# Optimization experiments

Measured on AMD Instinct MI355X. Metric: run time of the kernel, lower is better.

Reference implementation:

```python
import jax, jax.numpy as jnp
import numpy as np
import math

B, C, BINS, W = 2, 8, 1024, 512
HEADS = 16
HD = BINS // HEADS          # 64 head dim
ROT = BINS // HEADS // 2    # 32 rotated dims
EXP = 4
EPS = 1e-5
MAX_FREQ = 10.0


def setup_inputs() -> dict:
    key = jax.random.key(0)
    ks = jax.random.split(key, 8)
    def u(k, shape, fan_in):
        lim = 1.0 / math.sqrt(fan_in)
        return jax.random.uniform(k, shape, jnp.float32, -lim, lim)
    return {
        "x": jax.random.normal(ks[0], (B, C, BINS, W), jnp.float32),
        "norm1_w": jnp.ones((BINS,), jnp.float32),
        "norm1_b": jnp.zeros((BINS,), jnp.float32),
        # 'pixel' rotary init: linspace(1, max_freq/2, dim//2) * pi (learned)
        "rot_freqs": jnp.linspace(1.0, MAX_FREQ / 2, ROT // 2, dtype=jnp.float32) * math.pi,
        "q_w": u(ks[1], (C, BINS, BINS), BINS),
        "out_w": u(ks[2], (C, BINS, BINS), BINS),
        "norm2_w": jnp.ones((BINS,), jnp.float32),
        "norm2_b": jnp.zeros((BINS,), jnp.float32),
        "lin1_w": u(ks[3], (C, BINS * EXP, BINS), BINS),
        "lin2_w": u(ks[4], (C, BINS, BINS * EXP), BINS * EXP),
    }


def _mlin(x, w):
    # x: [b,c,f_in,w]; w: [c,f_out,f_in] -> [b,c,f_out,w]
    return jnp.einsum('bcfw,cgf->bcgw', x, w)


def _frame_norm(x, w, b):
    # LayerNorm over the bins axis (axis=2) of [b,c,bins,w]
    m = jnp.mean(x, axis=2, keepdims=True)
    v = jnp.var(x, axis=2, keepdims=True)
    xn = (x - m) * jax.lax.rsqrt(v + EPS)
    return xn * w[:, None] + b[:, None]


def _rotate(q, cos, sin):
    # q: [b,c,h,w,d]; rotate first ROT dims with interleaved-pair rotate_half
    q1, q2 = q[..., :ROT], q[..., ROT:]
    qp = q1.reshape(*q1.shape[:-1], ROT // 2, 2)
    rh = jnp.stack([-qp[..., 1], qp[..., 0]], axis=-1).reshape(q1.shape)
    return jnp.concatenate([q1 * cos + rh * sin, q2], axis=-1)


def _attention(x, rot_freqs, q_w, out_w):
    b, c, bins, w = x.shape
    # faithful to source: q, k, v ALL use q_proj
    y = _mlin(x, q_w)  # [b,c,bins,w]
    # -> [b,c,h,w,d]
    y = y.transpose(0, 1, 3, 2).reshape(b, c, w, HEADS, HD).transpose(0, 1, 3, 2, 4)
    # rotary angles: t * freqs, repeat-interleaved x2 -> [w, ROT]
    t = jnp.arange(w, dtype=jnp.float32)
    ang = jnp.repeat(t[:, None] * rot_freqs[None, :], 2, axis=-1)
    cos, sin = jnp.cos(ang), jnp.sin(ang)
    q = _rotate(y, cos, sin)
    k = _rotate(y, cos, sin)
    v = y
    # NOTE: source scales by 1/sqrt(h) where h == bins (spectral height)
    scores = jnp.einsum('bchwd,bchud->bchwu', q, k) / math.sqrt(bins)
    a = jnp.einsum('bchwu,bchud->bchwd', jax.nn.softmax(scores, axis=-1), v)
    # [b,c,h,w,d] -> [b,c,bins,w]
    a = a.transpose(0, 1, 3, 2, 4).reshape(b, c, w, bins).transpose(0, 1, 3, 2)
    return _mlin(a, out_w)


def reference(x, norm1_w, norm1_b, rot_freqs, q_w, out_w,
              norm2_w, norm2_b, lin1_w, lin2_w):
    z = _frame_norm(x, norm1_w, norm1_b)
    z = _attention(z, rot_freqs, q_w, out_w)
    x = x + z  # dropout=0 -> identity
    z = _frame_norm(x, norm2_w, norm2_b)
    z = _mlin(jax.nn.gelu(_mlin(z, lin1_w), approximate=False), lin2_w)
    return x + z
```

## Files before the change

kernel.cpp:

```cpp
#include <hip/hip_runtime.h>
#include <math.h>

#define BB 2
#define CCH 8
#define BINS 1024
#define WW 512
#define HEADS 16
#define HD 64
#define ROTD 32
#define EXPF 4
#define NXE 8388608L
#define NTW 32

typedef unsigned short ushortT;
typedef short bf16x8 __attribute__((ext_vector_type(8)));
typedef float f32x4 __attribute__((ext_vector_type(4)));

__device__ __forceinline__ ushortT f2bf(float f) {
    unsigned int u = __float_as_uint(f);
    u = (u + 0x7FFF + ((u >> 16) & 1)) >> 16;
    return (ushortT)u;
}
__device__ __forceinline__ float bf2f(ushortT h) {
    return __uint_as_float(((unsigned int)h) << 16);
}
__device__ __forceinline__ unsigned int cvtpk(float lo, float hi) {
    unsigned int r;
    asm("v_cvt_pk_bf16_f32 %0, %1, %2" : "=v"(r) : "v"(lo), "v"(hi));
    return r;
}
__device__ __forceinline__ float geluf(float x) {
    return 0.5f * x * (1.f + erff(x * 0.70710678118654752f));
}
__device__ __forceinline__ void gl_lds16(const ushortT* g, ushortT* l) {
    __builtin_amdgcn_global_load_lds(
        (const __attribute__((address_space(1))) unsigned int*)g,
        (__attribute__((address_space(3))) unsigned int*)l, 16, 0, 0);
}

__global__ __launch_bounds__(256)
void wcast_k(const float* __restrict__ s, ushortT* __restrict__ d, long n)
{
    long i = ((long)blockIdx.x * 256 + threadIdx.x) * 8;
    if (i >= n) return;
    float4 a = *(const float4*)&s[i];
    float4 b = *(const float4*)&s[i + 4];
    uint4 v;
    v.x = cvtpk(a.x, a.y); v.y = cvtpk(a.z, a.w);
    v.z = cvtpk(b.x, b.y); v.w = cvtpk(b.z, b.w);
    *(uint4*)&d[i] = v;
}

__global__ __launch_bounds__(1024)
void normT_k(const float* __restrict__ X, const float* __restrict__ wgt,
             const float* __restrict__ bia, ushortT* __restrict__ YT)
{
    __shared__ float tile[NTW][BINS + 1];
    __shared__ float red0[32][NTW], red1[32][NTW];
    __shared__ float ms[NTW], is[NTW];
    const int bc = blockIdx.x >> 4;
    const int w0 = (blockIdx.x & 15) * NTW;
    const int tid = threadIdx.x;
    const int w  = tid & (NTW - 1);
    const int fy = tid >> 5;
    const float* Xb = X + (long)bc * BINS * WW + w0;
    float s = 0.f, s2 = 0.f;
    for (int f = fy; f < BINS; f += 32) {
        float v = Xb[(long)f * WW + w];
        s += v; s2 += v * v;
        tile[w][f] = v;
    }
    red0[fy][w] = s; red1[fy][w] = s2;
    __syncthreads();
    if (tid < NTW) {
        float ss = 0.f, qq = 0.f;
        #pragma unroll
        for (int j = 0; j < 32; ++j) { ss += red0[j][tid]; qq += red1[j][tid]; }
        float m = ss * (1.f / BINS);
        float var = qq * (1.f / BINS) - m * m;
        ms[tid] = m; is[tid] = rsqrtf(var + 1e-5f);
    }
    __syncthreads();
    const int w2 = tid >> 5;
    const int c  = tid & 31;
    float m = ms[w2], inv = is[w2];
    ushortT* Yb = YT + ((long)bc * WW + w0 + w2) * BINS;
    #pragma unroll
    for (int jj = 0; jj < 4; ++jj) {
        int f0 = jj * 256 + c * 8;
        union { ushortT h[8]; uint4 v; } r;
        #pragma unroll
        for (int e = 0; e < 8; ++e) {
            int f = f0 + e;
            float v = (tile[w2][f] - m) * inv * wgt[f] + bia[f];
            r.h[e] = f2bf(v);
        }
        *(uint4*)&Yb[f0] = r.v;
    }
}

__global__ void rope_tab_k(const float* __restrict__ freqs,
                           float* __restrict__ cosT, float* __restrict__ sinT)
{
    int idx = blockIdx.x * 256 + threadIdx.x;
    if (idx >= WW * 16) return;
    int w = idx >> 4, i = idx & 15;
    float ang = (float)w * freqs[i];
    cosT[idx] = cosf(ang);
    sinT[idx] = sinf(ang);
}

__global__ __launch_bounds__(256)
void mattn_k(const ushortT* __restrict__ rotT, const ushortT* __restrict__ yT,
             ushortT* __restrict__ oT)
{
    __shared__ ushortT Qs[64 * 64];
    __shared__ ushortT Ks[64 * 64];
    __shared__ ushortT Vs[64 * 72];
    __shared__ ushortT Ps[64 * 72];
    const int z = blockIdx.y;
    const int bc = z >> 4, h = z & 15;
    const int wq0 = blockIdx.x * 64;
    const int tid = threadIdx.x;
    const int wv = tid >> 6, l = tid & 63;
    const int lr = l & 15, lk = l >> 4;
    const long hbase = (long)bc * WW * 1024 + h * 64;

    #pragma unroll
    for (int p = 0; p < 2; ++p) {
        int r0 = p * 32 + wv * 8;
        int row = r0 + (l >> 3);
        int gs = (l & 7) ^ (row & 7);
        gl_lds16(rotT + hbase + (long)(wq0 + row) * 1024 + gs * 8, Qs + r0 * 64);
    }

    f32x4 oacc[4] = {};
    float mrow[4] = {-INFINITY, -INFINITY, -INFINITY, -INFINITY};
    float lrow[4] = {0.f, 0.f, 0.f, 0.f};

    for (int u0 = 0; u0 < WW; u0 += 64) {
        #pragma unroll
        for (int p = 0; p < 2; ++p) {
            int r0 = p * 32 + wv * 8;
            int row = r0 + (l >> 3);
            int gs = (l & 7) ^ (row & 7);
            gl_lds16(rotT + hbase + (long)(u0 + row) * 1024 + gs * 8, Ks + r0 * 64);
        }
        #pragma unroll
        for (int rep = 0; rep < 2; ++rep) {
            int ch = rep * 4 + wv;
            union { uint4 v; ushortT h8[8]; } tmp;
            tmp.v = *(const uint4*)(yT + hbase + (long)(u0 + l) * 1024 + ch * 8);
            #pragma unroll
            for (int j = 0; j < 8; ++j)
                Vs[(ch * 8 + j) * 72 + l] = tmp.h8[j];
        }
        __syncthreads();

        f32x4 sacc[4] = {};
        #pragma unroll
        for (int ko = 0; ko < 2; ++ko) {
            int ar = wv * 16 + lr;
            bf16x8 aq = *(const bf16x8*)&Qs[ar * 64 + (((ko * 4) + lk) ^ (ar & 7)) * 8];
            #pragma unroll
            for (int f = 0; f < 4; ++f) {
                int br = f * 16 + lr;
                bf16x8 bk = *(const bf16x8*)&Ks[br * 64 + (((ko * 4) + lk) ^ (br & 7)) * 8];
                sacc[f] = __builtin_amdgcn_mfma_f32_16x16x32_bf16(aq, bk, sacc[f], 0, 0, 0);
            }
        }

        #pragma unroll
        for (int rg = 0; rg < 4; ++rg) {
            float s0 = sacc[0][rg] * (1.f / 32.f);
            float s1 = sacc[1][rg] * (1.f / 32.f);
            float s2 = sacc[2][rg] * (1.f / 32.f);
            float s3 = sacc[3][rg] * (1.f / 32.f);
            float mx = fmaxf(fmaxf(s0, s1), fmaxf(s2, s3));
            mx = fmaxf(mx, __shfl_xor(mx, 1));
            mx = fmaxf(mx, __shfl_xor(mx, 2));
            mx = fmaxf(mx, __shfl_xor(mx, 4));
            mx = fmaxf(mx, __shfl_xor(mx, 8));
            float mnew = fmaxf(mrow[rg], mx);
            float al = __expf(mrow[rg] - mnew);
            float p0 = __expf(s0 - mnew), p1 = __expf(s1 - mnew);
            float p2 = __expf(s2 - mnew), p3 = __expf(s3 - mnew);
            float rs = p0 + p1 + p2 + p3;
            rs += __shfl_xor(rs, 1);
            rs += __shfl_xor(rs, 2);
            rs += __shfl_xor(rs, 4);
            rs += __shfl_xor(rs, 8);
            lrow[rg] = lrow[rg] * al + rs;
            mrow[rg] = mnew;
            oacc[0][rg] *= al; oacc[1][rg] *= al;
            oacc[2][rg] *= al; oacc[3][rg] *= al;
            int prow = wv * 16 + lk * 4 + rg;
            Ps[prow * 72 +  0 + lr] = f2bf(p0);
            Ps[prow * 72 + 16 + lr] = f2bf(p1);
            Ps[prow * 72 + 32 + lr] = f2bf(p2);
            Ps[prow * 72 + 48 + lr] = f2bf(p3);
        }
        asm volatile("s_waitcnt lgkmcnt(0)" ::: "memory");

        #pragma unroll
        for (int ko = 0; ko < 2; ++ko) {
            int ar = wv * 16 + lr;
            bf16x8 ap = *(const bf16x8*)&Ps[ar * 72 + ko * 32 + lk * 8];
            #pragma unroll
            for (int f = 0; f < 4; ++f) {
                bf16x8 bv = *(const bf16x8*)&Vs[(f * 16 + lr) * 72 + ko * 32 + lk * 8];
                oacc[f] = __builtin_amdgcn_mfma_f32_16x16x32_bf16(ap, bv, oacc[f], 0, 0, 0);
            }
        }
        __syncthreads();
    }

    #pragma unroll
    for (int rg = 0; rg < 4; ++rg) {
        float inv = 1.f / lrow[rg];
        int w = wq0 + wv * 16 + lk * 4 + rg;
        long b2 = (long)bc * WW * 1024 + (long)w * 1024 + h * 64;
        #pragma unroll
        for (int f = 0; f < 4; ++f)
            oT[b2 + f * 16 + lr] = f2bf(oacc[f][rg] * inv);
    }
}

#define QPHASE(QM, QN, STAGES, VMW)                                          \
  {                                                                          \
    bf16x8 a0_[4], a1_[4], b0_[2], b1_[2];                                   \
    _Pragma("unroll")                                                        \
    for (int i = 0; i < 4; ++i) {                                            \
        int ra = wr * 128 + QM * 64 + i * 16 + lrow;                         \
        a0_[i] = *(const bf16x8*)&As[ra * 64 + ((lk    ) ^ (ra & 7)) * 8];   \
        a1_[i] = *(const bf16x8*)&As[ra * 64 + ((lk + 4) ^ (ra & 7)) * 8];   \
    }                                                                        \
    _Pragma("unroll")                                                        \
    for (int j = 0; j < 2; ++j) {                                            \
        int rb = wc * 64 + QN * 32 + j * 16 + lrow;                          \
        b0_[j] = *(const bf16x8*)&Bs[rb * 64 + ((lk    ) ^ (rb & 7)) * 8];   \
        b1_[j] = *(const bf16x8*)&Bs[rb * 64 + ((lk + 4) ^ (rb & 7)) * 8];   \
    }                                                                        \
    STAGES;                                                                  \
    VMW;                                                                     \
    asm volatile("s_waitcnt lgkmcnt(0)" ::: "memory");                       \
    __builtin_amdgcn_s_barrier();                                            \
    __builtin_amdgcn_s_setprio(1);                                           \
    _Pragma("unroll")                                                        \
    for (int i = 0; i < 4; ++i)                                              \
        _Pragma("unroll")                                                    \
        for (int j = 0; j < 2; ++j)                                          \
            acc[QM * 4 + i][QN * 2 + j] =                                    \
                __builtin_amdgcn_mfma_f32_16x16x32_bf16(                     \
                    a0_[i], b0_[j], acc[QM * 4 + i][QN * 2 + j], 0, 0, 0);   \
    _Pragma("unroll")                                                        \
    for (int i = 0; i < 4; ++i)                                              \
        _Pragma("unroll")                                                    \
        for (int j = 0; j < 2; ++j)                                          \
            acc[QM * 4 + i][QN * 2 + j] =                                    \
                __builtin_amdgcn_mfma_f32_16x16x32_bf16(                     \
                    a1_[i], b1_[j], acc[QM * 4 + i][QN * 2 + j], 0, 0, 0);   \
    __builtin_amdgcn_s_setprio(0);                                           \
  }

template<bool HASRES, bool GELUF, bool TRANSOUT>
__global__ __launch_bounds__(512)
void gemm8_k(const ushortT* __restrict__ A, long sA, int aMod,
             const ushortT* __restrict__ B, long sB,
             void* __restrict__ Cp, long sC,
             const float* __restrict__ R, long sR,
             int M, int N, int K, int gx, int gy)
{
    __shared__ ushortT smem[65536];
    const int nwg = gridDim.x;
    const int bid = blockIdx.x;
    const int lid = (bid & 7) * (nwg >> 3) + (bid >> 3);
    const int x = lid % gx;
    const int y = (lid / gx) % gy;
    const int z = lid / (gx * gy);
    const ushortT* Ab = A + (long)(z % aMod) * sA + (long)y * 256 * K;
    const ushortT* Bb = B + (long)z * sB + (long)x * 256 * K;
    const int tid = threadIdx.x;
    const int wv = tid >> 6, l = tid & 63;
    const int lrow = l & 15, lk = l >> 4;
    const int wr = wv >> 2, wc = wv & 3;
    f32x4 acc[8][4] = {};
    const int NT = K >> 6;

    auto stageAh = [&](int T, int qm) {
        ushortT* D = smem + (T & 1) * 32768;
        const int k0 = T << 6;
        #pragma unroll
        for (int t = 0; t < 2; ++t) {
            int r0 = wv * 16 + t * 8;
            int gr0 = ((r0 & 64) << 1) + qm * 64 + (r0 & 63);
            int gr = gr0 + (l >> 3);
            int gs = (l & 7) ^ (gr & 7);
            gl_lds16(Ab + (long)gr * K + k0 + gs * 8, D + gr0 * 64);
        }
    };
    auto stageBh = [&](int T, int qn) {
        ushortT* D = smem + (T & 1) * 32768 + 16384;
        const int k0 = T << 6;
        #pragma unroll
        for (int t = 0; t < 2; ++t) {
            int r0 = wv * 16 + t * 8;
            int gr0 = ((r0 >> 5) << 6) + qn * 32 + (r0 & 31);
            int gr = gr0 + (l >> 3);
            int gs = (l & 7) ^ (gr & 7);
            gl_lds16(Bb + (long)gr * K + k0 + gs * 8, D + gr0 * 64);
        }
    };

    stageAh(0, 0); stageAh(0, 1); stageBh(0, 0); stageBh(0, 1);
    if (NT > 1) {
        stageAh(1, 0); stageBh(1, 0);
        asm volatile("s_waitcnt vmcnt(4)" ::: "memory");
    } else {
        asm volatile("s_waitcnt vmcnt(0)" ::: "memory");
    }
    __builtin_amdgcn_s_barrier();

    for (int T = 0; T < NT; ++T) {
        const ushortT* As = smem + (T & 1) * 32768;
        const ushortT* Bs = As + 16384;
        const bool s1 = (T + 1 < NT), s2 = (T + 2 < NT);
        QPHASE(0, 0, if (s1) stageAh(T + 1, 1), );
        QPHASE(0, 1, if (s1) stageBh(T + 1, 1), );
        QPHASE(1, 0, if (s2) stageAh(T + 2, 0), );
        QPHASE(1, 1, if (s2) stageBh(T + 2, 0),
               if (s2) { asm volatile("s_waitcnt vmcnt(4)" ::: "memory"); }
               else    { asm volatile("s_waitcnt vmcnt(0)" ::: "memory"); });
    }

    const int m0g = y * 256 + wr * 128, n0g = x * 256 + wc * 64;
    if (!TRANSOUT) {
        float* Cf = (float*)Cp + (long)z * sC;
        #pragma unroll
        for (int ip = 0; ip < 8; ++ip)
            #pragma unroll
            for (int j = 0; j < 4; ++j)
                #pragma unroll
                for (int rg = 0; rg < 4; ++rg) {
                    long m = m0g + ip * 16 + lk * 4 + rg;
                    long n = n0g + j * 16 + lrow;
                    float v = acc[ip][j][rg];
                    if (GELUF) v = geluf(v);
                    if (HASRES) v += R[(long)z * sR + m * N + n];
                    Cf[m * N + n] = v;
                }
    } else {
        __syncthreads();
        ushortT* Ts = smem + wv * 4096;
        ushortT* CT = (ushortT*)Cp + (long)z * sC;
        #pragma unroll
        for (int s = 0; s < 2; ++s) {
            #pragma unroll
            for (int i2 = 0; i2 < 4; ++i2)
                #pragma unroll
                for (int j = 0; j < 4; ++j)
                    #pragma unroll
                    for (int rg = 0; rg < 4; ++rg) {
                        int ml = i2 * 16 + lk * 4 + rg;
                        int nl = j * 16 + lrow;
                        float v = acc[s * 4 + i2][j][rg];
                        if (GELUF) v = geluf(v);
                        Ts[nl * 64 + (((ml >> 3) ^ (nl & 7)) << 3) + (ml & 7)] = f2bf(v);
                    }
            #pragma unroll
            for (int p = 0; p < 8; ++p) {
                int nl = p * 8 + (l >> 3), mc = l & 7;
                uint4 d = *(const uint4*)&Ts[nl * 64 + ((mc ^ (nl & 7)) << 3)];
                *(uint4*)&CT[(long)(n0g + nl) * M + m0g + s * 64 + mc * 8] = d;
            }
        }
    }
}

template<bool HASRES, bool GELUF, bool TRANSOUT>
__global__ __launch_bounds__(512)
void pgemm_k(const ushortT* __restrict__ A, long sA, int aMod,
             const ushortT* __restrict__ B, long sB,
             void* __restrict__ Cp, long sC,
             const float* __restrict__ R, long sR,
             int M, int N, int K, int gx, int gy)
{
    __shared__ ushortT smem[3 * 24576];
    const int nwg = gridDim.x;
    const int bid = blockIdx.x;
    const int lid = (bid & 7) * (nwg >> 3) + (bid >> 3);
    const int x = lid % gx;
    const int y = (lid / gx) % gy;
    const int z = lid / (gx * gy);
    const ushortT* Ab = A + (long)(z % aMod) * sA + (long)y * 128 * K;
    const ushortT* Bb = B + (long)z * sB + (long)x * 256 * K;
    const int tid = threadIdx.x;
    const int wv = tid >> 6, l = tid & 63;
    const int lrow = l & 15, lk = l >> 4;
    const int mb = (wv >> 2) * 64;
    const int nb = (wv & 3) * 64;
    f32x4 acc[4][4] = {};
    const int NT = K >> 6;

    auto stageA = [&](int T) {
        ushortT* As = smem + (T % 3) * 24576;
        const int k0 = T << 6;
        #pragma unroll
        for (int t = 0; t < 2; ++t) {
            int r0 = wv * 16 + t * 8;
            int row = r0 + (l >> 3);
            int gs = (l & 7) ^ (row & 7);
            gl_lds16(Ab + (long)row * K + k0 + gs * 8, As + r0 * 64);
        }
    };
    auto stageBh = [&](int T, int h) {
        ushortT* Bs = smem + (T % 3) * 24576 + 8192;
        const int k0 = T << 6;
        #pragma unroll
        for (int t = 0; t < 2; ++t) {
            int r0 = wv * 32 + (h * 2 + t) * 8;
            int row = r0 + (l >> 3);
            int gs = (l & 7) ^ (row & 7);
            gl_lds16(Bb + (long)row * K + k0 + gs * 8, Bs + r0 * 64);
        }
    };

    stageA(0); stageBh(0, 0); stageBh(0, 1);
    if (NT > 1) {
        stageA(1); stageBh(1, 0); stageBh(1, 1);
        asm volatile("s_waitcnt vmcnt(6)" ::: "memory");
    } else {
        asm volatile("s_waitcnt vmcnt(0)" ::: "memory");
    }
    __builtin_amdgcn_s_barrier();

    for (int T = 0; T < NT; ++T) {
        const ushortT* As = smem + (T % 3) * 24576;
        const ushortT* Bs = As + 8192;
        const bool s1 = (T + 1 < NT), s2 = (T + 2 < NT);

        {
            bf16x8 af[4], bg[4];
            #pragma unroll
            for (int i = 0; i < 4; ++i) {
                int ra = mb + i * 16 + lrow;
                af[i] = *(const bf16x8*)&As[ra * 64 + ((lk) ^ (ra & 7)) * 8];
                int rb = nb + i * 16 + lrow;
                bg[i] = *(const bf16x8*)&Bs[rb * 64 + ((lk) ^ (rb & 7)) * 8];
            }
            if (s2) { stageA(T + 2); stageBh(T + 2, 0); }
            asm volatile("s_waitcnt lgkmcnt(0)" ::: "memory");
            __builtin_amdgcn_s_barrier();
            __builtin_amdgcn_s_setprio(1);
            #pragma unroll
            for (int i = 0; i < 4; ++i)
                #pragma unroll
                for (int j = 0; j < 4; ++j)
                    acc[i][j] = __builtin_amdgcn_mfma_f32_16x16x32_bf16(
                        af[i], bg[j], acc[i][j], 0, 0, 0);
            __builtin_amdgcn_s_setprio(0);
        }
        {
            bf16x8 af[4], bg[4];
            #pragma unroll
            for (int i = 0; i < 4; ++i) {
                int ra = mb + i * 16 + lrow;
                af[i] = *(const bf16x8*)&As[ra * 64 + ((lk + 4) ^ (ra & 7)) * 8];
                int rb = nb + i * 16 + lrow;
                bg[i] = *(const bf16x8*)&Bs[rb * 64 + ((lk + 4) ^ (rb & 7)) * 8];
            }
            if (s2) stageBh(T + 2, 1);
            if (s1) {
                if (s2) { asm volatile("s_waitcnt vmcnt(6)" ::: "memory"); }
                else    { asm volatile("s_waitcnt vmcnt(0)" ::: "memory"); }
            }
            asm volatile("s_waitcnt lgkmcnt(0)" ::: "memory");
            __builtin_amdgcn_s_barrier();
            __builtin_amdgcn_s_setprio(1);
            #pragma unroll
            for (int i = 0; i < 4; ++i)
                #pragma unroll
                for (int j = 0; j < 4; ++j)
                    acc[i][j] = __builtin_amdgcn_mfma_f32_16x16x32_bf16(
                        af[i], bg[j], acc[i][j], 0, 0, 0);
            __builtin_amdgcn_s_setprio(0);
        }
    }

    const int m0g = y * 128 + mb, n0g = x * 256 + nb;
    if (!TRANSOUT) {
        float* Cf = (float*)Cp + (long)z * sC;
        #pragma unroll
        for (int i = 0; i < 4; ++i)
            #pragma unroll
            for (int j = 0; j < 4; ++j)
                #pragma unroll
                for (int rg = 0; rg < 4; ++rg) {
                    long m = m0g + i * 16 + lk * 4 + rg;
                    long n = n0g + j * 16 + lrow;
                    float v = acc[i][j][rg];
                    if (GELUF) v = geluf(v);
                    if (HASRES) v += R[(long)z * sR + m * N + n];
                    Cf[m * N + n] = v;
                }
    } else {
        __syncthreads();
        ushortT* Ts = smem + wv * 4096;
        #pragma unroll
        for (int i = 0; i < 4; ++i)
            #pragma unroll
            for (int j = 0; j < 4; ++j)
                #pragma unroll
                for (int rg = 0; rg < 4; ++rg) {
                    int ml = i * 16 + lk * 4 + rg;
                    int nl = j * 16 + lrow;
                    float v = acc[i][j][rg];
                    if (GELUF) v = geluf(v);
                    Ts[nl * 64 + (((ml >> 3) ^ (nl & 7)) << 3) + (ml & 7)] = f2bf(v);
                }
        __syncthreads();
        ushortT* CT = (ushortT*)Cp + (long)z * sC;
        #pragma unroll
        for (int p = 0; p < 8; ++p) {
            int nl = p * 8 + (l >> 3), mc = l & 7;
            uint4 d = *(const uint4*)&Ts[nl * 64 + ((mc ^ (nl & 7)) << 3)];
            *(uint4*)&CT[(long)(n0g + nl) * M + m0g + mc * 8] = d;
        }
    }
}

template<bool HASRES, bool GELUF, bool TRANSOUT, bool ROPE>
__global__ __launch_bounds__(256)
void fgemm_k(const float* __restrict__ A, long sA, int aMod,
             const ushortT* __restrict__ B, long sB,
             void* __restrict__ Cp, long sC,
             const float* __restrict__ R, long sR,
             ushortT* __restrict__ Crot,
             const float* __restrict__ cosT, const float* __restrict__ sinT,
             int M, int N, int K, int gx, int gy)
{
    __shared__ ushortT smem[2 * 8192];
    ushortT* As = smem;
    ushortT* Bs = smem + 8192;
    const int nwg = gridDim.x;
    const int bid = blockIdx.x;
    const int lid = (bid & 7) * (nwg >> 3) + (bid >> 3);
    const int x = lid % gx;
    const int y = (lid / gx) % gy;
    const int z = lid / (gx * gy);
    const float*   Ab = A + (long)(z % aMod) * sA + (long)y * 128 * K;
    const ushortT* Bb = B + (long)z * sB + (long)x * 128 * K;
    const int tid = threadIdx.x;
    const int wv = tid >> 6, l = tid & 63;
    const int lrow = l & 15, lk = l >> 4;
    const int mb = (wv >> 1) * 64, nb = (wv & 1) * 64;
    const int arow = tid >> 3, agrp = tid & 7;
    f32x4 acc[4][4] = {};
    float4 a0[4], a1[4];
    const int NT = K >> 6;

    auto fetchA = [&](int k0) {
        #pragma unroll
        for (int c = 0; c < 4; ++c) {
            const float* src = Ab + (long)(arow + c * 32) * K + k0 + agrp * 8;
            a0[c] = *(const float4*)src;
            a1[c] = *(const float4*)(src + 4);
        }
    };
    auto commitA = [&]() {
        #pragma unroll
        for (int c = 0; c < 4; ++c) {
            int row = arow + c * 32;
            uint4 v;
            v.x = cvtpk(a0[c].x, a0[c].y);
            v.y = cvtpk(a0[c].z, a0[c].w);
            v.z = cvtpk(a1[c].x, a1[c].y);
            v.w = cvtpk(a1[c].z, a1[c].w);
            *(uint4*)&As[row * 64 + ((agrp ^ (row & 7)) << 3)] = v;
        }
    };
    auto stageB = [&](int k0) {
        #pragma unroll
        for (int t = 0; t < 4; ++t) {
            int r0 = wv * 32 + t * 8;
            int row = r0 + (l >> 3);
            int gs = (l & 7) ^ (row & 7);
            gl_lds16(Bb + (long)row * K + k0 + gs * 8, Bs + r0 * 64);
        }
    };
    auto compute = [&]() {
        #pragma unroll
        for (int ko = 0; ko < 2; ++ko) {
            bf16x8 af[4], bg[4];
            #pragma unroll
            for (int i = 0; i < 4; ++i) {
                int ra = mb + i * 16 + lrow;
                af[i] = *(const bf16x8*)&As[ra * 64 + ((lk + ko * 4) ^ (ra & 7)) * 8];
                int rb = nb + i * 16 + lrow;
                bg[i] = *(const bf16x8*)&Bs[rb * 64 + ((lk + ko * 4) ^ (rb & 7)) * 8];
            }
            #pragma unroll
            for (int i = 0; i < 4; ++i)
                #pragma unroll
                for (int j = 0; j < 4; ++j)
                    acc[i][j] = __builtin_amdgcn_mfma_f32_16x16x32_bf16(
                        af[i], bg[j], acc[i][j], 0, 0, 0);
        }
    };

    fetchA(0);
    for (int t = 0; t < NT; ++t) {
        if (t > 0) __syncthreads();
        stageB(t << 6);
        commitA();
        if (t + 1 < NT) fetchA((t + 1) << 6);
        __syncthreads();
        compute();
    }

    const int m0g = y * 128 + mb, n0g = x * 128 + nb;
    if (!TRANSOUT) {
        float* Cf = (float*)Cp + (long)z * sC;
        #pragma unroll
        for (int i = 0; i < 4; ++i)
            #pragma unroll
            for (int j = 0; j < 4; ++j)
                #pragma unroll
                for (int rg = 0; rg < 4; ++rg) {
                    long m = m0g + i * 16 + lk * 4 + rg;
                    long n = n0g + j * 16 + lrow;
                    float v = acc[i][j][rg];
                    if (GELUF) v = geluf(v);
                    if (HASRES) v += R[(long)z * sR + m * N + n];
                    Cf[m * N + n] = v;
                }
    } else {
        ushortT* Ts = smem + wv * 4096;
        __syncthreads();
        #pragma unroll
        for (int i = 0; i < 4; ++i)
            #pragma unroll
            for (int j = 0; j < 4; ++j)
                #pragma unroll
                for (int rg = 0; rg < 4; ++rg) {
                    int ml = i * 16 + lk * 4 + rg;
                    int nl = j * 16 + lrow;
                    float v = acc[i][j][rg];
                    if (GELUF) v = geluf(v);
                    Ts[nl * 64 + (((ml >> 3) ^ (nl & 7)) << 3) + (ml & 7)] = f2bf(v);
                }
        __syncthreads();
        ushortT* CT = (ushortT*)Cp + (long)z * sC;
        #pragma unroll
        for (int p = 0; p < 8; ++p) {
            int nl = p * 8 + (l >> 3), mc = l & 7;
            uint4 d = *(const uint4*)&Ts[nl * 64 + ((mc ^ (nl & 7)) << 3)];
            int wg = n0g + nl;
            int g0 = m0g + mc * 8;
            *(uint4*)&CT[(long)wg * M + g0] = d;
            if (ROPE) {
                ushortT* RT = Crot + (long)z * sC;
                int d0 = g0 & 63;
                if (d0 >= ROTD) {
                    *(uint4*)&RT[(long)wg * M + g0] = d;
                } else {
                    union { uint4 v; ushortT h8[8]; } in, ov;
                    in.v = d;
                    #pragma unroll
                    for (int j = 0; j < 8; j += 2) {
                        int i2 = (d0 + j) >> 1;
                        float cc = cosT[wg * 16 + i2], ss = sinT[wg * 16 + i2];
                        float a = bf2f(in.h8[j]), b = bf2f(in.h8[j + 1]);
                        ov.h8[j]     = f2bf(a * cc - b * ss);
                        ov.h8[j + 1] = f2bf(b * cc + a * ss);
                    }
                    *(uint4*)&RT[(long)wg * M + g0] = ov.v;
                }
            }
        }
    }
}

extern "C" void kernel_launch(void* const* d_in, const int* in_sizes, int n_in,
                              void* d_out, int out_size, void* d_ws, size_t ws_size,
                              hipStream_t stream)
{
    const float* x    = (const float*)d_in[0];
    const float* n1w  = (const float*)d_in[1];
    const float* n1b  = (const float*)d_in[2];
    const float* freqs= (const float*)d_in[3];
    const float* qw   = (const float*)d_in[4];
    const float* ow   = (const float*)d_in[5];
    const float* n2w  = (const float*)d_in[6];
    const float* n2b  = (const float*)d_in[7];
    const float* l1w  = (const float*)d_in[8];
    const float* l2w  = (const float*)d_in[9];
    float* out = (float*)d_out;
    char* wsb  = (char*)d_ws;
    const long MB = 1L << 20;

    ushortT* znT  = (ushortT*)(wsb +   0 * MB);
    ushortT* yT   = (ushortT*)(wsb +  16 * MB);
    ushortT* rotT = (ushortT*)(wsb +  32 * MB);
    ushortT* CfT  = (ushortT*)(wsb +  48 * MB);
    ushortT* wB   = (ushortT*)(wsb +   0 * MB);
    ushortT* zn2T = (ushortT*)(wsb +  64 * MB);
    ushortT* h1T  = (ushortT*)(wsb +  80 * MB);
    float*   cosT = (float*)  (wsb + 144 * MB);
    float*   sinT = cosT + WW * 16;

    rope_tab_k<<<32, 256, 0, stream>>>(freqs, cosT, sinT);

    normT_k<<<BB * CCH * 16, 1024, 0, stream>>>(x, n1w, n1b, znT);

    fgemm_k<false, false, true, true><<<512, 256, 0, stream>>>(
        qw,  (long)BINS * BINS, CCH,
        znT, (long)WW * BINS,
        yT,  (long)WW * BINS,
        nullptr, 0,
        rotT, cosT, sinT,
        BINS, WW, BINS, 4, 8);

    mattn_k<<<dim3(8, 256), 256, 0, stream>>>(rotT, yT, CfT);

    fgemm_k<true, false, false, false><<<512, 256, 0, stream>>>(
        ow,  (long)BINS * BINS, CCH,
        CfT, (long)WW * BINS,
        out, (long)BINS * WW,
        x,   (long)BINS * WW,
        nullptr, nullptr, nullptr,
        BINS, WW, BINS, 4, 8);

    wcast_k<<<16384, 256, 0, stream>>>(l1w, wB, 8L * BINS * EXPF * BINS);

    normT_k<<<BB * CCH * 16, 1024, 0, stream>>>(out, n2w, n2b, zn2T);

    gemm8_k<false, true, true><<<512, 512, 0, stream>>>(
        wB,   (long)BINS * EXPF * BINS, CCH,
        zn2T, (long)WW * BINS,
        h1T,  (long)WW * BINS * EXPF,
        nullptr, 0,
        BINS * EXPF, WW, BINS, 2, 16);

    wcast_k<<<16384, 256, 0, stream>>>(l2w, wB, 8L * BINS * EXPF * BINS);

    pgemm_k<true, false, false><<<256, 512, 0, stream>>>(
        wB,  (long)BINS * BINS * EXPF, CCH,
        h1T, (long)WW * BINS * EXPF,
        out, (long)BINS * WW,
        out, (long)BINS * WW,
        BINS, WW, BINS * EXPF, 2, 8);
}
```

Baseline: 428.8 us.

## Fold weight casts into attention and MLP1 GEMM epilogues

Measured after the change: 426.5 us. Within noise of the previous version (-0.5%).

```diff
diff --git a/kernel.cpp b/kernel.cpp
--- a/kernel.cpp
+++ b/kernel.cpp
@@ -37,18 +37,13 @@
         (const __attribute__((address_space(1))) unsigned int*)g,
         (__attribute__((address_space(3))) unsigned int*)l, 16, 0, 0);
 }
-
-__global__ __launch_bounds__(256)
-void wcast_k(const float* __restrict__ s, ushortT* __restrict__ d, long n)
-{
-    long i = ((long)blockIdx.x * 256 + threadIdx.x) * 8;
-    if (i >= n) return;
-    float4 a = *(const float4*)&s[i];
-    float4 b = *(const float4*)&s[i + 4];
+__device__ __forceinline__ void cast8(const float* s, ushortT* d) {
+    float4 a = *(const float4*)s;
+    float4 b = *(const float4*)(s + 4);
     uint4 v;
     v.x = cvtpk(a.x, a.y); v.y = cvtpk(a.z, a.w);
     v.z = cvtpk(b.x, b.y); v.w = cvtpk(b.z, b.w);
-    *(uint4*)&d[i] = v;
+    *(uint4*)d = v;
 }
 
 __global__ __launch_bounds__(1024)
@@ -112,7 +107,8 @@
 
 __global__ __launch_bounds__(256)
 void mattn_k(const ushortT* __restrict__ rotT, const ushortT* __restrict__ yT,
-             ushortT* __restrict__ oT)
+             ushortT* __restrict__ oT,
+             const float* __restrict__ wsrc, ushortT* __restrict__ wdst)
 {
     __shared__ ushortT Qs[64 * 64];
     __shared__ ushortT Ks[64 * 64];
@@ -223,6 +219,15 @@
         #pragma unroll
         for (int f = 0; f < 4; ++f)
             oT[b2 + f * 16 + lr] = f2bf(oacc[f][rg] * inv);
+    }
+
+    if (wsrc) {
+        long wbase = ((long)z * 8 + blockIdx.x) * 16384 + tid * 8;
+        #pragma unroll
+        for (int p = 0; p < 8; ++p) {
+            long i = wbase + (long)p * 2048;
+            cast8(wsrc + i, wdst + i);
+        }
     }
 }
 
@@ -269,6 +274,7 @@
              const ushortT* __restrict__ B, long sB,
              void* __restrict__ Cp, long sC,
              const float* __restrict__ R, long sR,
+             const float* __restrict__ wsrc, ushortT* __restrict__ wdst,
              int M, int N, int K, int gx, int gy)
 {
     __shared__ ushortT smem[65536];
@@ -373,6 +379,15 @@
                 uint4 d = *(const uint4*)&Ts[nl * 64 + ((mc ^ (nl & 7)) << 3)];
                 *(uint4*)&CT[(long)(n0g + nl) * M + m0g + s * 64 + mc * 8] = d;
             }
+        }
+    }
+
+    if (wsrc) {
+        long wbase = (long)bid * 65536 + tid * 8;
+        #pragma unroll
+        for (int p = 0; p < 16; ++p) {
+            long i = wbase + (long)p * 4096;
+            cast8(wsrc + i, wdst + i);
         }
     }
 }
@@ -703,10 +718,11 @@
     ushortT* yT   = (ushortT*)(wsb +  16 * MB);
     ushortT* rotT = (ushortT*)(wsb +  32 * MB);
     ushortT* CfT  = (ushortT*)(wsb +  48 * MB);
-    ushortT* wB   = (ushortT*)(wsb +   0 * MB);
     ushortT* zn2T = (ushortT*)(wsb +  64 * MB);
     ushortT* h1T  = (ushortT*)(wsb +  80 * MB);
-    float*   cosT = (float*)  (wsb + 144 * MB);
+    ushortT* wB1  = (ushortT*)(wsb + 144 * MB);
+    ushortT* wB2  = (ushortT*)(wsb +   0 * MB);
+    float*   cosT = (float*)  (wsb + 208 * MB);
     float*   sinT = cosT + WW * 16;
 
     rope_tab_k<<<32, 256, 0, stream>>>(freqs, cosT, sinT);
@@ -721,7 +737,7 @@
         rotT, cosT, sinT,
         BINS, WW, BINS, 4, 8);
 
-    mattn_k<<<dim3(8, 256), 256, 0, stream>>>(rotT, yT, CfT);
+    mattn_k<<<dim3(8, 256), 256, 0, stream>>>(rotT, yT, CfT, l1w, wB1);
 
     fgemm_k<true, false, false, false><<<512, 256, 0, stream>>>(
         ow,  (long)BINS * BINS, CCH,
@@ -731,21 +747,18 @@
         nullptr, nullptr, nullptr,
         BINS, WW, BINS, 4, 8);
 
-    wcast_k<<<16384, 256, 0, stream>>>(l1w, wB, 8L * BINS * EXPF * BINS);
-
     normT_k<<<BB * CCH * 16, 1024, 0, stream>>>(out, n2w, n2b, zn2T);
 
     gemm8_k<false, true, true><<<512, 512, 0, stream>>>(
-        wB,   (long)BINS * EXPF * BINS, CCH,
+        wB1,  (long)BINS * EXPF * BINS, CCH,
         zn2T, (long)WW * BINS,
         h1T,  (long)WW * BINS * EXPF,
         nullptr, 0,
+        l2w, wB2,
         BINS * EXPF, WW, BINS, 2, 16);
 
-    wcast_k<<<16384, 256, 0, stream>>>(l2w, wB, 8L * BINS * EXPF * BINS);
-
     pgemm_k<true, false, false><<<256, 512, 0, stream>>>(
-        wB,  (long)BINS * BINS * EXPF, CCH,
+        wB2, (long)BINS * BINS * EXPF, CCH,
         h1T, (long)WW * BINS * EXPF,
         out, (long)BINS * WW,
         out, (long)BINS * WW,
```
